# Performance work log

Hardware: AMD Instinct MI355X
Metric: run time of the kernel (lower is better)

The kernel has to match this reference:

```python
import jax, jax.numpy as jnp
import numpy as np
import math

B, C, H, W = 2, 256, 64, 64
E = 256           # embed_dim
AE = 64           # angle embed dim = embed_dim // 4
NH = 3            # num angle hypotheses
HEADS = 8
HALF = AE // 2    # 32 sin/cos frequencies

# 3x3 kernel tap grid (dy, dx), row-major, matching torchvision DeformConv2d tap order
KY = jnp.array([-1,-1,-1, 0,0,0, 1,1,1], jnp.float32)
KX = jnp.array([-1, 0, 1,-1,0,1,-1,0,1], jnp.float32)
# assumed angle hypothesis deltas around the predicted angle
HYPO_DELTAS = (-math.pi/12, 0.0, math.pi/12)


def conv2d(x, w, b, pad):
    y = jax.lax.conv_general_dilated(x, w, (1, 1), [(pad, pad), (pad, pad)],
                                     dimension_numbers=('NCHW', 'OIHW', 'NCHW'))
    return y + b[None, :, None, None]


def gen_offsets(angles):
    """Rotate the base 3x3 kernel taps by the per-pixel angle; offset = rotated - base.
    angles: (B, H*W, 1) -> offsets (B, 18, H, W), (dy,dx) interleaved per tap."""
    a = angles.reshape(-1, H, W)
    c = jnp.cos(a)[..., None]           # (B,H,W,1)
    s = jnp.sin(a)[..., None]
    ry = KX * s + KY * c                # rotated y of each tap, (B,H,W,9)
    rx = KX * c - KY * s                # rotated x
    off = jnp.stack([ry - KY, rx - KX], axis=-1)   # (B,H,W,9,2)
    return off.reshape(-1, H, W, 18).transpose(0, 3, 1, 2)


def deform_conv(x, offsets, w, b):
    """DeformConv2d k=3, stride=1, pad=1, dilation=1, zero padding outside.
    x (B,C,H,W), offsets (B,18,H,W), w (O,C,3,3)."""
    off = offsets.reshape(x.shape[0], 9, 2, H, W)
    oy = off[:, :, 0].transpose(0, 2, 3, 1)          # (B,H,W,9)
    ox = off[:, :, 1].transpose(0, 2, 3, 1)
    hh = jnp.arange(H, dtype=jnp.float32)[None, :, None, None]
    ww = jnp.arange(W, dtype=jnp.float32)[None, None, :, None]
    py = hh + KY + oy                                # sample y, (B,H,W,9)
    px = ww + KX + ox
    y0 = jnp.floor(py)
    x0 = jnp.floor(px)
    wy = (py - y0)[:, None]                          # (B,1,H,W,9)
    wx = (px - x0)[:, None]

    def gather(yi, xi):
        valid = (yi >= 0) & (yi <= H - 1) & (xi >= 0) & (xi <= W - 1)
        yc = jnp.clip(yi, 0, H - 1).astype(jnp.int32)
        xc = jnp.clip(xi, 0, W - 1).astype(jnp.int32)
        g = jax.vmap(lambda img, yy, xx: img[:, yy, xx])(x, yc, xc)  # (B,C,H,W,9)
        return g * valid[:, None].astype(x.dtype)

    samp = (gather(y0, x0) * (1 - wy) * (1 - wx)
            + gather(y0, x0 + 1) * (1 - wy) * wx
            + gather(y0 + 1, x0) * wy * (1 - wx)
            + gather(y0 + 1, x0 + 1) * wy * wx)      # (B,C,H,W,9)
    w9 = w.reshape(w.shape[0], w.shape[1], 9)
    return jnp.einsum('bchwk,ock->bohw', samp, w9) + b[None, :, None, None]


def angle_encode(angles, freq_mult, w1, b1, ln_g, ln_b, w2, b2):
    an = (angles / (math.pi / 2))[..., 0]                       # (B,HW) le90 norm
    dim_t = jnp.arange(HALF, dtype=jnp.float32) / HALF * math.pi
    ae = an[..., None] * (freq_mult * dim_t)                    # (B,HW,HALF)
    emb = jnp.concatenate([jnp.sin(ae), jnp.cos(ae)], axis=-1)  # (B,HW,AE)
    h = emb @ w1.T + b1
    mu = h.mean(-1, keepdims=True)
    var = h.var(-1, keepdims=True)
    h = (h - mu) * jax.lax.rsqrt(var + 1e-5) * ln_g + ln_b
    return jax.nn.relu(h) @ w2.T + b2


def mha(q, kv, in_w, in_b, out_w, out_b):
    # q (L,1,E), kv (L,NH,E); torch nn.MultiheadAttention math
    wq, wk, wv = jnp.split(in_w, 3, axis=0)
    bq, bk, bv = jnp.split(in_b, 3)
    hd = E // HEADS
    Q = (q @ wq.T + bq).reshape(-1, 1, HEADS, hd).transpose(0, 2, 1, 3)
    K = (kv @ wk.T + bk).reshape(-1, NH, HEADS, hd).transpose(0, 2, 1, 3)
    V = (kv @ wv.T + bv).reshape(-1, NH, HEADS, hd).transpose(0, 2, 1, 3)
    attn = jax.nn.softmax(jnp.einsum('lhqd,lhkd->lhqk', Q, K) / math.sqrt(hd), axis=-1)
    o = jnp.einsum('lhqk,lhkd->lhqd', attn, V).transpose(0, 2, 1, 3).reshape(-1, 1, E)
    return o @ out_w.T + out_b


def group_norm(x, g, b, groups=32, eps=1e-5):
    Bq, Cc, Hh, Ww = x.shape
    xg = x.reshape(Bq, groups, Cc // groups, Hh, Ww)
    mu = xg.mean((2, 3, 4), keepdims=True)
    var = xg.var((2, 3, 4), keepdims=True)
    xn = ((xg - mu) * jax.lax.rsqrt(var + eps)).reshape(x.shape)
    return xn * g[None, :, None, None] + b[None, :, None, None]


def setup_inputs() -> dict:
    key = jax.random.key(0)
    ks = iter(jax.random.split(key, 32))
    r = lambda *s: jax.random.normal(next(ks), s, jnp.float32) * 0.05
    z = lambda *s: jnp.zeros(s, jnp.float32)
    return {
        'features': jax.random.normal(next(ks), (B, C, H, W), jnp.float32),
        'ap_w1': r(C // 4, C, 3, 3), 'ap_b1': z(C // 4),
        'ap_w2': r(1, C // 4, 1, 1), 'ap_b2': z(1),
        'freq_mult': jnp.ones((HALF,), jnp.float32),
        'ae_w1': r(AE, AE), 'ae_b1': z(AE),
        'ae_ln_g': jnp.ones((AE,), jnp.float32), 'ae_ln_b': z(AE),
        'ae_w2': r(AE, AE), 'ae_b2': z(AE),
        'dc_w': r(E, C, 3, 3), 'dc_b': z(E),
        'attn_in_w': r(3 * E, E), 'attn_in_b': z(3 * E),
        'attn_out_w': r(E, E), 'attn_out_b': z(E),
        'ja_w1': r(E, E + AE, 1, 1), 'ja_b1': z(E),
        'ja_w2': r(E, E, 1, 1), 'ja_b2': z(E),
        'op_w1': r(E, E, 3, 3), 'op_b1': z(E),
        'gn_g': jnp.ones((E,), jnp.float32), 'gn_b': z(E),
        'op_w2': r(E, E, 1, 1), 'op_b2': z(E),
    }


def reference(features, ap_w1, ap_b1, ap_w2, ap_b2, freq_mult, ae_w1, ae_b1,
              ae_ln_g, ae_ln_b, ae_w2, ae_b2, dc_w, dc_b, attn_in_w, attn_in_b,
              attn_out_w, attn_out_b, ja_w1, ja_b1, ja_w2, ja_b2, op_w1, op_b1,
              gn_g, gn_b, op_w2, op_b2):
    # 1) angle prediction
    h1 = jax.nn.relu(conv2d(features, ap_w1, ap_b1, 1))
    angles = conv2d(h1, ap_w2, ap_b2, 0).reshape(B, H * W, 1)
    # 2) periodic angle encoding
    angle_embed = angle_encode(angles, freq_mult, ae_w1, ae_b1, ae_ln_g, ae_ln_b, ae_w2, ae_b2)
    # 3) rotation-aware deformable alignment
    aligned = deform_conv(features, gen_offsets(angles), dc_w, dc_b)
    # 4) multi-angle hypotheses fused by per-pixel attention
    cand = [deform_conv(features, gen_offsets(angles + d), dc_w, dc_b) for d in HYPO_DELTAS]
    feat_stack = jnp.stack(cand, axis=1)                       # (B,NH,E,H,W)
    q = aligned.transpose(0, 2, 3, 1).reshape(B * H * W, 1, E)
    kv = feat_stack.transpose(0, 3, 4, 1, 2).reshape(B * H * W, NH, E)
    fused = mha(q, kv, attn_in_w, attn_in_b, attn_out_w, attn_out_b)
    fused = fused.reshape(B, H, W, E).transpose(0, 3, 1, 2)
    # 5) joint angle-spatial attention gate
    ae_sp = angle_embed.reshape(B, H, W, AE).transpose(0, 3, 1, 2)
    ji = jnp.concatenate([fused, ae_sp], axis=1)
    gate = jax.nn.sigmoid(conv2d(jax.nn.relu(conv2d(ji, ja_w1, ja_b1, 0)), ja_w2, ja_b2, 0))
    enh = fused * gate + fused
    # 6) output projection
    o = jax.nn.relu(group_norm(conv2d(enh, op_w1, op_b1, 1), gn_g, gn_b))
    return conv2d(o, op_w2, op_b2, 0)
```

## Files before the change

kernel.cpp:

```cpp
#include <hip/hip_runtime.h>

#define PI_F 3.14159265358979323846f
#define HWSZ 4096
#define NPIX 8192

typedef __attribute__((ext_vector_type(8))) short short8;
typedef __attribute__((ext_vector_type(4))) short short4_t;
typedef __attribute__((ext_vector_type(4))) float f32x4;

__device__ __forceinline__ short f2bf(float x){
  unsigned u = __float_as_uint(x);
  unsigned r = (u + 0x7FFFu + ((u >> 16) & 1u)) >> 16;
  return (short)r;
}
__device__ __forceinline__ float bf2f(short v){
  return __uint_as_float(((unsigned)(unsigned short)v) << 16);
}

__device__ __forceinline__ float wsum64(float v){
  #pragma unroll
  for (int m = 32; m >= 1; m >>= 1) v += __shfl_xor(v, m, 64);
  return v;
}
__device__ __forceinline__ float wsum8(float v){
  v += __shfl_xor(v, 1, 64);
  v += __shfl_xor(v, 2, 64);
  v += __shfl_xor(v, 4, 64);
  return v;
}

__device__ __forceinline__ void gl_lds(const short* g, short* s){
  __builtin_amdgcn_global_load_lds(
      (const __attribute__((address_space(1))) unsigned int*)g,
      (__attribute__((address_space(3))) unsigned int*)s, 16, 0, 0);
}

__global__ void k_zero4(short* __restrict__ p, int n4){
  int i = blockIdx.x*256 + threadIdx.x;
  if (i < n4) ((short4_t*)p)[i] = (short4_t){0,0,0,0};
}

__global__ void k_nchw_split(const float* __restrict__ in, short* __restrict__ feat_bf,
    short* __restrict__ A3){
  __shared__ float tile[32][33];
  int b = blockIdx.z;
  int p0 = blockIdx.x * 32, c0 = blockIdx.y * 32;
  int tx = threadIdx.x, ty = threadIdx.y;
  #pragma unroll
  for (int i = ty; i < 32; i += 8)
    tile[i][tx] = in[((size_t)b*256 + c0 + i)*HWSZ + p0 + tx];
  __syncthreads();
  #pragma unroll
  for (int i = ty; i < 32; i += 8){
    float x = tile[tx][i];
    short hi = f2bf(x);
    short lo = f2bf(x - bf2f(hi));
    size_t p = (size_t)b*HWSZ + p0 + i;
    feat_bf[p*256 + c0 + tx] = hi;
    A3[p*768 + c0 + tx] = hi;
    A3[p*768 + 256 + c0 + tx] = hi;
    A3[p*768 + 512 + c0 + tx] = lo;
  }
}

__global__ void k_prep_tapw(const float* __restrict__ w, short* __restrict__ Bm){
  __shared__ short tile[9][256];
  int o = blockIdx.x;
  const float* wo = w + (size_t)o*2304;
  for (int i = threadIdx.x; i < 2304; i += 256){
    int c = i / 9, k = i - c*9;
    tile[k][c] = f2bf(wo[i]);
  }
  __syncthreads();
  for (int i = threadIdx.x; i < 2304; i += 256){
    int k = i >> 8, c = i & 255;
    Bm[((size_t)(k*256 + o))*256 + c] = tile[k][c];
  }
}

__global__ void k_prep_igw(const float* __restrict__ w, short* __restrict__ B2){
  __shared__ short tile[2304];
  int o = blockIdx.x;
  const float* wo = w + (size_t)o*2304;
  for (int i = threadIdx.x; i < 2304; i += 256){
    int c = i / 9, k = i - c*9;
    tile[k*256 + c] = f2bf(wo[i]);
  }
  __syncthreads();
  short* out = B2 + (size_t)o*2304;
  for (int i = threadIdx.x; i < 2304; i += 256) out[i] = tile[i];
}

__global__ void k_prep_apw3(const float* __restrict__ w, short* __restrict__ B3){
  int n = blockIdx.x, c = threadIdx.x;
  short hi = 0, lo = 0;
  if (n < 576){
    int o = n & 63, k = n >> 6;
    float x = w[((size_t)o*256 + c)*9 + k];
    hi = f2bf(x);
    lo = f2bf(x - bf2f(hi));
  }
  B3[(size_t)n*768 + c] = hi;
  B3[(size_t)n*768 + 256 + c] = lo;
  B3[(size_t)n*768 + 512 + c] = hi;
}

__global__ void k_castall(const float* __restrict__ s0, const float* __restrict__ s1,
    const float* __restrict__ s2, const float* __restrict__ s3, const float* __restrict__ s4,
    short* __restrict__ d0, short* __restrict__ d1, short* __restrict__ d2,
    short* __restrict__ d3, short* __restrict__ d4){
  int i = blockIdx.x*256 + threadIdx.x;
  if (i < 196608) d0[i] = f2bf(s0[i]);
  else if (i < 262144) d1[i-196608] = f2bf(s1[i-196608]);
  else if (i < 344064) d2[i-262144] = f2bf(s2[i-262144]);
  else if (i < 409600) d3[i-344064] = f2bf(s3[i-344064]);
  else if (i < 475136) d4[i-409600] = f2bf(s4[i-409600]);
}

template<int EPI, int BM>
__global__ __launch_bounds__(256) void k_gemml(const short* __restrict__ A,
    const short* __restrict__ B, void* __restrict__ Cv,
    const float* __restrict__ bias, const short* __restrict__ aux,
    int K, int ldc){
  constexpr int WM = BM/2;
  constexpr int AF = WM/16;
  __shared__ alignas(16) short sA[2][BM*32];
  __shared__ alignas(16) short sB[2][128*32];
  int tid = threadIdx.x;
  int w = tid >> 6, l = tid & 63;
  int wr = w & 1, wc = w >> 1;
  int ml = l & 15, g = l >> 4;
  int srow = tid >> 2;
  int sch = (tid & 3)*8;
  int m0 = blockIdx.x*BM, n0 = blockIdx.y*128;
  const short* Agp = A + (size_t)(m0 + srow)*K + sch;
  const short* Bgp = B + (size_t)(n0 + srow)*K + sch;
  short* sAd = &sA[0][srow*32 + sch];
  short* sBd = &sB[0][srow*32 + sch];
  f32x4 acc[AF][4];
  #pragma unroll
  for (int i = 0; i < AF; ++i)
    #pragma unroll
    for (int j = 0; j < 4; ++j) acc[i][j] = (f32x4){0.f,0.f,0.f,0.f};

  #define STAGE(bf, kt) { \
    _Pragma("unroll") \
    for (int c = 0; c < BM/64; ++c) \
      gl_lds(Agp + (size_t)(c*64)*K + (kt)*32, sAd + (bf)*BM*32 + c*2048); \
    _Pragma("unroll") \
    for (int c = 0; c < 2; ++c) \
      gl_lds(Bgp + (size_t)(c*64)*K + (kt)*32, sBd + (bf)*4096 + c*2048); \
  }
  int nk = K >> 5;
  STAGE(0, 0)
  int buf = 0;
  for (int kt = 0; kt < nk; ++kt){
    __syncthreads();
    if (kt + 1 < nk){ STAGE(buf^1, kt+1) }
    short8 af[AF], bq[4];
    #pragma unroll
    for (int i = 0; i < AF; ++i)
      af[i] = *(const short8*)&sA[buf][(wr*WM + i*16 + ml)*32 + g*8];
    #pragma unroll
    for (int j = 0; j < 4; ++j)
      bq[j] = *(const short8*)&sB[buf][(wc*64 + j*16 + ml)*32 + g*8];
    #pragma unroll
    for (int i = 0; i < AF; ++i)
      #pragma unroll
      for (int j = 0; j < 4; ++j)
        acc[i][j] = __builtin_amdgcn_mfma_f32_16x16x32_bf16(af[i], bq[j], acc[i][j], 0, 0, 0);
    buf ^= 1;
  }
  #undef STAGE

  int m0w = m0 + wr*WM;
  int n0w = n0 + wc*64;
  if constexpr (EPI == 4){
    __shared__ float cst[BM][129];
    #pragma unroll
    for (int fm = 0; fm < AF; ++fm)
      #pragma unroll
      for (int fn = 0; fn < 4; ++fn)
        #pragma unroll
        for (int r = 0; r < 4; ++r){
          int cl = wc*64 + fn*16 + ml;
          cst[wr*WM + fm*16 + g*4 + r][cl] = acc[fm][fn][r] + bias[blockIdx.y*128 + cl];
        }
    __syncthreads();
    int px0 = blockIdx.x*BM;
    int b = px0 >> 12, hw0 = px0 & 4095;
    int o = tid >> 1, seg = (tid & 1)*(BM/2);
    float* op = (float*)Cv + (((size_t)(b*256 + blockIdx.y*128 + o)) << 12) + hw0 + seg;
    #pragma unroll
    for (int i = 0; i < BM/2; i += 4){
      float4 vv = {cst[seg+i][o], cst[seg+i+1][o], cst[seg+i+2][o], cst[seg+i+3][o]};
      *(float4*)(op + i) = vv;
    }
  } else {
    #pragma unroll
    for (int fm = 0; fm < AF; ++fm)
      #pragma unroll
      for (int fn = 0; fn < 4; ++fn)
        #pragma unroll
        for (int r = 0; r < 4; ++r){
          int row = m0w + fm*16 + g*4 + r;
          int col = n0w + fn*16 + ml;
          float v = acc[fm][fn][r];
          if constexpr (EPI == 0){
            ((short*)Cv)[(size_t)row*ldc + col] = f2bf(v);
          } else if constexpr (EPI == 1){
            ((short*)Cv)[(size_t)row*ldc + col] = f2bf(v + bias[col]);
          } else if constexpr (EPI == 2){
            ((short*)Cv)[(size_t)row*ldc + col] = f2bf(fmaxf(v + bias[col], 0.f));
          } else if constexpr (EPI == 3){
            float f = bf2f(aux[(size_t)row*320 + col]);
            float s = 1.f/(1.f + __expf(-(v + bias[col])));
            ((short*)Cv)[(size_t)row*ldc + col] = f2bf(f * (1.f + s));
          } else if constexpr (EPI == 6){
            float f = bf2f(aux[(size_t)row*320 + col]);
            float s = 1.f/(1.f + __expf(-(v + bias[col])));
            int b = row >> 12, hw = row & 4095;
            int pi = b*4356 + ((hw>>6)+1)*66 + (hw&63) + 1;
            ((short*)Cv)[(size_t)pi*256 + col] = f2bf(f * (1.f + s));
          } else if constexpr (EPI == 7){
            ((short*)Cv)[(size_t)(col>>8)*2097152 + (size_t)row*256 + (col&255)] = f2bf(v);
          } else {
            ((float*)Cv)[(size_t)row*ldc + col] = v;
          }
        }
  }
}

__global__ __launch_bounds__(256) void k_igconv(const short* __restrict__ Xpad,
    const short* __restrict__ B2, float* __restrict__ PG){
  __shared__ alignas(16) short sA[2][64*32];
  __shared__ alignas(16) short sB[2][128*32];
  int zg = blockIdx.z;
  int tid = threadIdx.x;
  int w = tid >> 6, l = tid & 63;
  int wr = w & 1, wc = w >> 1;
  int ml = l & 15, g = l >> 4;
  int srow = tid >> 2;
  int sch = (tid & 3)*8;
  int m0 = blockIdx.x*64, n0 = blockIdx.y*128;
  int b = blockIdx.x >> 6, imgrow = blockIdx.x & 63;
  int qbase = b*4356 + (imgrow+1)*66 + srow + 1;
  const short* Bgp = B2 + (size_t)(n0 + srow)*2304 + zg*768 + sch;
  short* sAd = &sA[0][srow*32 + sch];
  short* sBd = &sB[0][srow*32 + sch];
  int toff[3];
  #pragma unroll
  for (int i = 0; i < 3; ++i){
    int t = zg*3 + i;
    toff[i] = (t/3 - 1)*66 + (t%3) - 1;
  }
  f32x4 acc[2][4];
  #pragma unroll
  for (int i = 0; i < 2; ++i)
    #pragma unroll
    for (int j = 0; j < 4; ++j) acc[i][j] = (f32x4){0.f,0.f,0.f,0.f};

  #define STG(bf, kt) { \
    int tap = (kt) >> 3, cofs = ((kt) & 7)*32; \
    gl_lds(Xpad + (size_t)(qbase + toff[tap])*256 + cofs + sch, sAd + (bf)*2048); \
    gl_lds(Bgp + (kt)*32, sBd + (bf)*4096); \
    gl_lds(Bgp + (size_t)64*2304 + (kt)*32, sBd + (bf)*4096 + 2048); \
  }
  STG(0, 0)
  int buf = 0;
  for (int kt = 0; kt < 24; ++kt){
    __syncthreads();
    if (kt < 23){ STG(buf^1, kt+1) }
    short8 af[2], bq[4];
    #pragma unroll
    for (int i = 0; i < 2; ++i)
      af[i] = *(const short8*)&sA[buf][(wr*32 + i*16 + ml)*32 + g*8];
    #pragma unroll
    for (int j = 0; j < 4; ++j)
      bq[j] = *(const short8*)&sB[buf][(wc*64 + j*16 + ml)*32 + g*8];
    #pragma unroll
    for (int i = 0; i < 2; ++i)
      #pragma unroll
      for (int j = 0; j < 4; ++j)
        acc[i][j] = __builtin_amdgcn_mfma_f32_16x16x32_bf16(af[i], bq[j], acc[i][j], 0, 0, 0);
    buf ^= 1;
  }
  #undef STG

  float* out = PG + (size_t)zg*2097152;
  int m0w = m0 + wr*32;
  int n0w = n0 + wc*64;
  #pragma unroll
  for (int fm = 0; fm < 2; ++fm)
    #pragma unroll
    for (int fn = 0; fn < 4; ++fn)
      #pragma unroll
      for (int r = 0; r < 4; ++r){
        int row = m0w + fm*16 + g*4 + r;
        int col = n0w + fn*16 + ml;
        out[(size_t)row*256 + col] = acc[fm][fn][r];
      }
}

__global__ void k_aph1enc(const float* __restrict__ T, const float* __restrict__ b1,
    const float* __restrict__ w2, const float* __restrict__ b2,
    const float* __restrict__ freq,
    const float* __restrict__ ew1, const float* __restrict__ eb1,
    const float* __restrict__ lng, const float* __restrict__ lnb,
    const float* __restrict__ ew2, const float* __restrict__ eb2,
    float* __restrict__ ang, short* __restrict__ gateA){
  const int KYi[9] = {-1,-1,-1,0,0,0,1,1,1};
  const int KXi[9] = {-1,0,1,-1,0,1,-1,0,1};
  int lane = threadIdx.x & 63;
  int p = blockIdx.x*4 + (threadIdx.x >> 6);
  int hw = p & 4095;
  int h = hw >> 6, w = hw & 63;
  float acc = b1[lane];
  #pragma unroll
  for (int k = 0; k < 9; ++k){
    int y = h + KYi[k], x = w + KXi[k];
    if (y < 0 || y > 63 || x < 0 || x > 63) continue;
    acc += T[(size_t)(p + KYi[k]*64 + KXi[k])*640 + k*64 + lane];
  }
  float av = wsum64(fmaxf(acc, 0.f) * w2[lane]) + b2[0];
  if (lane == 0) ang[p] = av;
  float an = av * (2.0f / PI_F);
  int f = lane & 31;
  float ph = an * freq[f] * ((float)f * (PI_F / 32.0f));
  float emb = (lane < 32) ? __sinf(ph) : __cosf(ph);
  float hh = eb1[lane];
  const float* w1r = ew1 + lane*64;
  #pragma unroll 8
  for (int i = 0; i < 64; ++i){
    float e = __shfl(emb, i, 64);
    hh = fmaf(e, w1r[i], hh);
  }
  float mu = wsum64(hh) * (1.0f/64.0f);
  float d = hh - mu;
  float var = wsum64(d*d) * (1.0f/64.0f);
  float hn = fmaf(d * rsqrtf(var + 1e-5f), lng[lane], lnb[lane]);
  float r = fmaxf(hn, 0.f);
  float o = eb2[lane];
  const float* w2r = ew2 + lane*64;
  #pragma unroll 8
  for (int i = 0; i < 64; ++i){
    float e = __shfl(r, i, 64);
    o = fmaf(e, w2r[i], o);
  }
  gateA[(size_t)p*320 + 256 + lane] = f2bf(o);
}

__global__ void k_meta(const float* __restrict__ ang, int2* __restrict__ moff,
    float4* __restrict__ mw){
  int i = blockIdx.x*256 + threadIdx.x;
  if (i >= NPIX*27) return;
  int p = i / 27;
  int j = i - p*27;
  int hyp = j / 9;
  int tap = j - hyp*9;
  float ky = (float)(tap/3 - 1), kx = (float)(tap - (tap/3)*3 - 1);
  float a = ang[p] + ((float)hyp - 1.0f) * (PI_F / 12.0f);
  float sn = __sinf(a), cs = __cosf(a);
  int b = p >> 12, hw = p & 4095;
  float py = (float)(hw >> 6) + kx*sn + ky*cs;
  float px = (float)(hw & 63) + kx*cs - ky*sn;
  float y0f = floorf(py), x0f = floorf(px);
  float wy = py - y0f, wx = px - x0f;
  int y0 = (int)y0f, x0 = (int)x0f;
  bool vx0 = (unsigned)x0 < 64u, vx1 = (unsigned)(x0+1) < 64u;
  bool vy0 = (unsigned)y0 < 64u, vy1 = (unsigned)(y0+1) < 64u;
  int xb = vx0 ? x0 : (vx1 ? x0+1 : 0);
  float sx0 = vx0 ? 1.f-wx : (vx1 ? wx : 0.f);
  float sx1 = (vx0 && vx1) ? wx : 0.f;
  int ry0 = vy0 ? y0 : 0;
  int ry1 = vy1 ? y0+1 : 0;
  float vw0 = vy0 ? 1.f-wy : 0.f;
  float vw1 = vy1 ? wy : 0.f;
  int base = (b << 12);
  moff[i] = make_int2(tap*4194304 + (base + ry0*64 + xb)*512,
                      tap*4194304 + (base + ry1*64 + xb)*512);
  mw[i] = make_float4(vw0*sx0, vw0*sx1, vw1*sx0, vw1*sx1);
}

__global__ __launch_bounds__(256, 4) void k_sample(const short* __restrict__ G,
    const int2* __restrict__ moff, const float4* __restrict__ mw,
    const float* __restrict__ bias, short* __restrict__ cand){
  __shared__ int2 smo[216];
  __shared__ float4 smw[216];
  int id = blockIdx.x;
  int sw = (id & 7)*128 + (id >> 3);
  int tid = threadIdx.x;
  int pbase = sw*8;
  if (tid < 216){
    smo[tid] = moff[pbase*27 + tid];
    smw[tid] = mw[pbase*27 + tid];
  }
  __syncthreads();
  int lp = (tid >> 6)*2 + ((tid >> 5) & 1);
  int p = pbase + lp;
  int c8 = (tid & 31)*8;
  float av[3][8];
  {
    float4 b0 = *(const float4*)(bias + c8);
    float4 b1 = *(const float4*)(bias + c8 + 4);
    #pragma unroll
    for (int h2 = 0; h2 < 3; ++h2){
      av[h2][0]=b0.x; av[h2][1]=b0.y; av[h2][2]=b0.z; av[h2][3]=b0.w;
      av[h2][4]=b1.x; av[h2][5]=b1.y; av[h2][6]=b1.z; av[h2][7]=b1.w;
    }
  }
  #pragma unroll
  for (int hyp = 0; hyp < 3; ++hyp){
    #pragma unroll 3
    for (int tap = 0; tap < 9; ++tap){
      int idx = lp*27 + hyp*9 + tap;
      int2 o = smo[idx];
      float4 wv = smw[idx];
      const short* r0 = (const short*)((const char*)G + o.x) + c8;
      const short* r1 = (const short*)((const char*)G + o.y) + c8;
      short8 v00 = *(const short8*)r0;
      short8 v01 = *(const short8*)(r0 + 256);
      short8 v10 = *(const short8*)r1;
      short8 v11 = *(const short8*)(r1 + 256);
      #pragma unroll
      for (int e = 0; e < 8; ++e){
        float s = wv.x*bf2f(v00[e]) + wv.y*bf2f(v01[e]);
        s += wv.z*bf2f(v10[e]) + wv.w*bf2f(v11[e]);
        av[hyp][e] += s;
      }
    }
  }
  #pragma unroll
  for (int hyp = 0; hyp < 3; ++hyp){
    short8 o;
    #pragma unroll
    for (int e = 0; e < 8; ++e) o[e] = f2bf(av[hyp][e]);
    *(short8*)(cand + ((size_t)hyp*NPIX + p)*256 + c8) = o;
  }
}

__global__ void k_attn(const short* __restrict__ Q, const short* __restrict__ KV,
    short* __restrict__ O){
  int lane = threadIdx.x & 63;
  int p = blockIdx.x*4 + (threadIdx.x >> 6);
  float q[4];
  { short4_t t = *(const short4_t*)(Q + (size_t)p*256 + lane*4);
    #pragma unroll
    for (int j = 0; j < 4; ++j) q[j] = bf2f(t[j]); }
  float kv[3][2][4];
  #pragma unroll
  for (int i = 0; i < 3; ++i){
    const short* rp = KV + (size_t)(i*NPIX + p)*512 + lane*4;
    short4_t kt = *(const short4_t*)rp;
    short4_t vt = *(const short4_t*)(rp + 256);
    #pragma unroll
    for (int j = 0; j < 4; ++j){ kv[i][0][j] = bf2f(kt[j]); kv[i][1][j] = bf2f(vt[j]); }
  }
  const float sc = 0.17677669529663688f;
  float s[3];
  #pragma unroll
  for (int i = 0; i < 3; ++i){
    float d = 0.f;
    #pragma unroll
    for (int j = 0; j < 4; ++j) d = fmaf(q[j], kv[i][0][j], d);
    s[i] = wsum8(d) * sc;
  }
  float m = fmaxf(s[0], fmaxf(s[1], s[2]));
  float e0 = __expf(s[0]-m), e1 = __expf(s[1]-m), e2 = __expf(s[2]-m);
  float inv = 1.f/(e0+e1+e2);
  short4_t ot;
  #pragma unroll
  for (int j = 0; j < 4; ++j)
    ot[j] = f2bf((e0*kv[0][1][j] + e1*kv[1][1][j] + e2*kv[2][1][j]) * inv);
  *(short4_t*)(O + (size_t)p*256 + lane*4) = ot;
}

__global__ void k_sum3stat(const float* __restrict__ PG, const float* __restrict__ bias,
    float* __restrict__ t, float* __restrict__ spart){
  int p0 = blockIdx.x * 8;
  int c = threadIdx.x;
  float bb = bias[c];
  float s = 0.f, s2 = 0.f;
  #pragma unroll
  for (int pp = 0; pp < 8; ++pp){
    size_t idx = (size_t)(p0+pp)*256 + c;
    float v = PG[idx] + PG[idx + 2097152] + PG[idx + 4194304] + bb;
    t[idx] = v;
    s += v; s2 = fmaf(v, v, s2);
  }
  s  += __shfl_xor(s, 1, 64);  s  += __shfl_xor(s, 2, 64);  s  += __shfl_xor(s, 4, 64);
  s2 += __shfl_xor(s2, 1, 64); s2 += __shfl_xor(s2, 2, 64); s2 += __shfl_xor(s2, 4, 64);
  if ((c & 7) == 0){
    int b = p0 >> 12;
    int bg = b*32 + (c >> 3);
    int blk = blockIdx.x & 511;
    spart[(size_t)(bg*512 + blk)*2]     = s;
    spart[(size_t)(bg*512 + blk)*2 + 1] = s2;
  }
}

__global__ void k_gnfin(const float* __restrict__ spart, float* __restrict__ stat){
  int bg = blockIdx.x;
  const float* sp = spart + (size_t)bg*1024;
  float s = 0.f, s2 = 0.f;
  for (int i = threadIdx.x; i < 512; i += 256){
    s += sp[i*2]; s2 += sp[i*2+1];
  }
  s = wsum64(s); s2 = wsum64(s2);
  __shared__ float rs[4], rs2[4];
  int wid = threadIdx.x >> 6;
  if ((threadIdx.x & 63) == 0){ rs[wid] = s; rs2[wid] = s2; }
  __syncthreads();
  if (threadIdx.x == 0){
    float S = rs[0]+rs[1]+rs[2]+rs[3];
    float S2 = rs2[0]+rs2[1]+rs2[2]+rs2[3];
    float mean = S * (1.f/32768.f);
    float var = S2 * (1.f/32768.f) - mean*mean;
    stat[bg*2]   = mean;
    stat[bg*2+1] = rsqrtf(var + 1e-5f);
  }
}

__global__ void k_gnrelu(const float* __restrict__ t, const float* __restrict__ stat,
    const float* __restrict__ gng, const float* __restrict__ gnb,
    short* __restrict__ a){
  int p = blockIdx.x*4 + (threadIdx.x >> 6);
  int c4 = (threadIdx.x & 63)*4;
  int b = p >> 12, g = c4 >> 3;
  float mean = stat[(b*32+g)*2], rstd = stat[(b*32+g)*2+1];
  float4 gg = *(const float4*)(gng + c4);
  float4 bb = *(const float4*)(gnb + c4);
  float4 v = *(const float4*)(t + (size_t)p*256 + c4);
  short4_t o;
  o[0] = f2bf(fmaxf((v.x - mean)*rstd*gg.x + bb.x, 0.f));
  o[1] = f2bf(fmaxf((v.y - mean)*rstd*gg.y + bb.y, 0.f));
  o[2] = f2bf(fmaxf((v.z - mean)*rstd*gg.z + bb.z, 0.f));
  o[3] = f2bf(fmaxf((v.w - mean)*rstd*gg.w + bb.w, 0.f));
  *(short4_t*)(a + (size_t)p*256 + c4) = o;
}

extern "C" void kernel_launch(void* const* d_in, const int* in_sizes, int n_in,
                              void* d_out, int out_size, void* d_ws, size_t ws_size,
                              hipStream_t stream){
  (void)in_sizes; (void)n_in; (void)out_size; (void)ws_size;
  const float* features   = (const float*)d_in[0];
  const float* ap_w1      = (const float*)d_in[1];
  const float* ap_b1      = (const float*)d_in[2];
  const float* ap_w2      = (const float*)d_in[3];
  const float* ap_b2      = (const float*)d_in[4];
  const float* freq       = (const float*)d_in[5];
  const float* ae_w1      = (const float*)d_in[6];
  const float* ae_b1      = (const float*)d_in[7];
  const float* ae_ln_g    = (const float*)d_in[8];
  const float* ae_ln_b    = (const float*)d_in[9];
  const float* ae_w2      = (const float*)d_in[10];
  const float* ae_b2      = (const float*)d_in[11];
  const float* dc_w       = (const float*)d_in[12];
  const float* dc_b       = (const float*)d_in[13];
  const float* attn_in_w  = (const float*)d_in[14];
  const float* attn_in_b  = (const float*)d_in[15];
  const float* attn_out_w = (const float*)d_in[16];
  const float* attn_out_b = (const float*)d_in[17];
  const float* ja_w1      = (const float*)d_in[18];
  const float* ja_b1      = (const float*)d_in[19];
  const float* ja_w2      = (const float*)d_in[20];
  const float* ja_b2      = (const float*)d_in[21];
  const float* op_w1      = (const float*)d_in[22];
  const float* op_b1      = (const float*)d_in[23];
  const float* gn_g       = (const float*)d_in[24];
  const float* gn_b       = (const float*)d_in[25];
  const float* op_w2      = (const float*)d_in[26];
  const float* op_b2      = (const float*)d_in[27];

  char* base = (char*)d_ws;
  #define ALLOC(ty, name, elems) ty* name = (ty*)base; base += (size_t)(elems)*sizeof(ty);
  ALLOC(short, feat_bf, 8192*256)
  ALLOC(short, Bdc,     2304*256)
  ALLOC(short, B2op,    256*2304)
  ALLOC(short, B3ap,    640*768)
  ALLOC(short, inw_bf,  768*256)
  ALLOC(short, wot_bf,  256*256)
  ALLOC(short, jw1_bf,  256*320)
  ALLOC(short, jw2_bf,  256*256)
  ALLOC(short, wop2_bf, 256*256)
  ALLOC(short, Gbuf,    24576*768)
  ALLOC(short, gguard,  64)
  ALLOC(short, cand_bf, 3*8192*256)
  ALLOC(short, O_bf,    8192*256)
  ALLOC(short, gateA,   8192*320)
  ALLOC(short, hid_bf,  8192*256)
  ALLOC(short, enh_pad, 2*4356*256)
  ALLOC(float, angbuf,  8192)
  ALLOC(float, tbuf,    8192*256)
  ALLOC(float, gstat,   128)
  ALLOC(float, spart,   65536)
  ALLOC(short, a_bf,    8192*256)
  ALLOC(int,   moffb,   2*NPIX*27)
  ALLOC(float, mwb,     4*NPIX*27)
  #undef ALLOC
  (void)gguard;
  short* A3 = cand_bf;
  float* T_ap = (float*)Gbuf;
  short* KVbuf = Gbuf;
  short* Qbuf  = Gbuf + (size_t)24576*512;
  float* PG    = (float*)Gbuf;
  int2*  moff  = (int2*)moffb;
  float4* mwv  = (float4*)mwb;

  dim3 t32(32, 8);
  k_zero4<<<2178, 256, 0, stream>>>(enh_pad, 557568);
  k_nchw_split<<<dim3(128,8,2), t32, 0, stream>>>(features, feat_bf, A3);
  k_prep_tapw<<<256, 256, 0, stream>>>(dc_w,  Bdc);
  k_prep_igw<<<256, 256, 0, stream>>>(op_w1, B2op);
  k_prep_apw3<<<640, 256, 0, stream>>>(ap_w1, B3ap);
  k_castall<<<1856, 256, 0, stream>>>(attn_in_w, attn_out_w, ja_w1, ja_w2, op_w2,
                                      inw_bf, wot_bf, jw1_bf, jw2_bf, wop2_bf);

  k_gemml<5,64><<<dim3(128,5), 256, 0, stream>>>(A3, B3ap, T_ap, nullptr, nullptr, 768, 640);
  k_aph1enc<<<2048, 256, 0, stream>>>(T_ap, ap_b1, ap_w2, ap_b2, freq,
                                      ae_w1, ae_b1, ae_ln_g, ae_ln_b, ae_w2, ae_b2,
                                      angbuf, gateA);
  k_meta<<<864, 256, 0, stream>>>(angbuf, moff, mwv);
  k_gemml<7,128><<<dim3(64,18), 256, 0, stream>>>(feat_bf, Bdc, Gbuf, nullptr, nullptr, 256, 2304);
  k_sample<<<1024, 256, 0, stream>>>(Gbuf, moff, mwv, dc_b, cand_bf);
  k_gemml<1,128><<<dim3(192,4), 256, 0, stream>>>(cand_bf, inw_bf + (size_t)256*256, KVbuf,
                                                  attn_in_b + 256, nullptr, 256, 512);
  k_gemml<1,64><<<dim3(128,2), 256, 0, stream>>>(cand_bf + (size_t)NPIX*256, inw_bf, Qbuf,
                                                 attn_in_b, nullptr, 256, 256);
  k_attn<<<2048, 256, 0, stream>>>(Qbuf, KVbuf, O_bf);
  k_gemml<1,64><<<dim3(128,2), 256, 0, stream>>>(O_bf, wot_bf, gateA, attn_out_b, nullptr, 256, 320);
  k_gemml<2,64><<<dim3(128,2), 256, 0, stream>>>(gateA, jw1_bf, hid_bf, ja_b1, nullptr, 320, 256);
  k_gemml<6,64><<<dim3(128,2), 256, 0, stream>>>(hid_bf, jw2_bf, enh_pad, ja_b2, gateA, 256, 256);
  k_igconv<<<dim3(128,2,3), 256, 0, stream>>>(enh_pad, B2op, PG);
  k_sum3stat<<<1024, 256, 0, stream>>>(PG, op_b1, tbuf, spart);
  k_gnfin<<<64, 256, 0, stream>>>(spart, gstat);
  k_gnrelu<<<2048, 256, 0, stream>>>(tbuf, gstat, gn_g, gn_b, a_bf);
  k_gemml<4,64><<<dim3(128,2), 256, 0, stream>>>(a_bf, wop2_bf, (float*)d_out, op_b2, nullptr, 256, 256);
}
```

Baseline: 218.9 us.

## Merge prep kernels, fuse meta into encoder, shrink angle GEMM K, retile small GEMMs

Five weight-prep and zeroing kernels become one launch, and the per-pixel offset/weight metadata computation moves into the angle-encoder kernel so the angle buffer round trip and one launch go away. The angle-predictor GEMM drops from a three-term to a two-term split-bf16 product (hi*hi + lo*hi), which shrinks K from 768 to 512. The small N=256 GEMMs use a 64-wide N tile to double the block count for better occupancy. Dropping the hi*lo term lowers the precision of the predicted angle, and that loss carries into the sampling offsets.

```diff
diff --git a/kernel.cpp b/kernel.cpp
--- a/kernel.cpp
+++ b/kernel.cpp
@@ -35,9 +35,57 @@
       (__attribute__((address_space(3))) unsigned int*)s, 16, 0, 0);
 }
 
-__global__ void k_zero4(short* __restrict__ p, int n4){
-  int i = blockIdx.x*256 + threadIdx.x;
-  if (i < n4) ((short4_t*)p)[i] = (short4_t){0,0,0,0};
+__global__ void k_prep(const float* __restrict__ dc_w, const float* __restrict__ op_w1,
+    const float* __restrict__ ap_w1,
+    const float* __restrict__ s0, const float* __restrict__ s1,
+    const float* __restrict__ s2, const float* __restrict__ s3, const float* __restrict__ s4,
+    short* __restrict__ enh_pad, short* __restrict__ Bdc, short* __restrict__ B2op,
+    short* __restrict__ B3, short* __restrict__ d0, short* __restrict__ d1,
+    short* __restrict__ d2, short* __restrict__ d3, short* __restrict__ d4){
+  __shared__ short tile[2304];
+  int bx = blockIdx.x, tid = threadIdx.x;
+  if (bx < 2178){
+    int i = bx*256 + tid;
+    if (i < 557568) ((short4_t*)enh_pad)[i] = (short4_t){0,0,0,0};
+  } else if (bx < 2434){
+    int o = bx - 2178;
+    const float* wo = dc_w + (size_t)o*2304;
+    for (int i = tid; i < 2304; i += 256){
+      int c = i / 9, k = i - c*9;
+      tile[k*256 + c] = f2bf(wo[i]);
+    }
+    __syncthreads();
+    for (int i = tid; i < 2304; i += 256){
+      int k = i >> 8, c = i & 255;
+      Bdc[((size_t)(k*256 + o))*256 + c] = tile[i];
+    }
+  } else if (bx < 2690){
+    int o = bx - 2434;
+    const float* wo = op_w1 + (size_t)o*2304;
+    for (int i = tid; i < 2304; i += 256){
+      int c = i / 9, k = i - c*9;
+      tile[k*256 + c] = f2bf(wo[i]);
+    }
+    __syncthreads();
+    short* out = B2op + (size_t)o*2304;
+    for (int i = tid; i < 2304; i += 256) out[i] = tile[i];
+  } else if (bx < 3330){
+    int n = bx - 2690, c = tid;
+    short hi = 0;
+    if (n < 576){
+      int o = n & 63, k = n >> 6;
+      hi = f2bf(ap_w1[((size_t)o*256 + c)*9 + k]);
+    }
+    B3[(size_t)n*512 + c] = hi;
+    B3[(size_t)n*512 + 256 + c] = hi;
+  } else {
+    int i = (bx - 3330)*256 + tid;
+    if (i < 196608) d0[i] = f2bf(s0[i]);
+    else if (i < 262144) d1[i-196608] = f2bf(s1[i-196608]);
+    else if (i < 344064) d2[i-262144] = f2bf(s2[i-262144]);
+    else if (i < 409600) d3[i-344064] = f2bf(s3[i-344064]);
+    else if (i < 475136) d4[i-409600] = f2bf(s4[i-409600]);
+  }
 }
 
 __global__ void k_nchw_split(const float* __restrict__ in, short* __restrict__ feat_bf,
@@ -57,82 +105,29 @@
     short lo = f2bf(x - bf2f(hi));
     size_t p = (size_t)b*HWSZ + p0 + i;
     feat_bf[p*256 + c0 + tx] = hi;
-    A3[p*768 + c0 + tx] = hi;
-    A3[p*768 + 256 + c0 + tx] = hi;
-    A3[p*768 + 512 + c0 + tx] = lo;
-  }
-}
-
-__global__ void k_prep_tapw(const float* __restrict__ w, short* __restrict__ Bm){
-  __shared__ short tile[9][256];
-  int o = blockIdx.x;
-  const float* wo = w + (size_t)o*2304;
-  for (int i = threadIdx.x; i < 2304; i += 256){
-    int c = i / 9, k = i - c*9;
-    tile[k][c] = f2bf(wo[i]);
-  }
-  __syncthreads();
-  for (int i = threadIdx.x; i < 2304; i += 256){
-    int k = i >> 8, c = i & 255;
-    Bm[((size_t)(k*256 + o))*256 + c] = tile[k][c];
-  }
-}
-
-__global__ void k_prep_igw(const float* __restrict__ w, short* __restrict__ B2){
-  __shared__ short tile[2304];
-  int o = blockIdx.x;
-  const float* wo = w + (size_t)o*2304;
-  for (int i = threadIdx.x; i < 2304; i += 256){
-    int c = i / 9, k = i - c*9;
-    tile[k*256 + c] = f2bf(wo[i]);
-  }
-  __syncthreads();
-  short* out = B2 + (size_t)o*2304;
-  for (int i = threadIdx.x; i < 2304; i += 256) out[i] = tile[i];
-}
-
-__global__ void k_prep_apw3(const float* __restrict__ w, short* __restrict__ B3){
-  int n = blockIdx.x, c = threadIdx.x;
-  short hi = 0, lo = 0;
-  if (n < 576){
-    int o = n & 63, k = n >> 6;
-    float x = w[((size_t)o*256 + c)*9 + k];
-    hi = f2bf(x);
-    lo = f2bf(x - bf2f(hi));
-  }
-  B3[(size_t)n*768 + c] = hi;
-  B3[(size_t)n*768 + 256 + c] = lo;
-  B3[(size_t)n*768 + 512 + c] = hi;
-}
-
-__global__ void k_castall(const float* __restrict__ s0, const float* __restrict__ s1,
-    const float* __restrict__ s2, const float* __restrict__ s3, const float* __restrict__ s4,
-    short* __restrict__ d0, short* __restrict__ d1, short* __restrict__ d2,
-    short* __restrict__ d3, short* __restrict__ d4){
-  int i = blockIdx.x*256 + threadIdx.x;
-  if (i < 196608) d0[i] = f2bf(s0[i]);
-  else if (i < 262144) d1[i-196608] = f2bf(s1[i-196608]);
-  else if (i < 344064) d2[i-262144] = f2bf(s2[i-262144]);
-  else if (i < 409600) d3[i-344064] = f2bf(s3[i-344064]);
-  else if (i < 475136) d4[i-409600] = f2bf(s4[i-409600]);
-}
-
-template<int EPI, int BM>
+    A3[p*512 + c0 + tx] = hi;
+    A3[p*512 + 256 + c0 + tx] = lo;
+  }
+}
+
+template<int EPI, int BM, int BN = 128>
 __global__ __launch_bounds__(256) void k_gemml(const short* __restrict__ A,
     const short* __restrict__ B, void* __restrict__ Cv,
     const float* __restrict__ bias, const short* __restrict__ aux,
     int K, int ldc){
-  constexpr int WM = BM/2;
+  constexpr int NWC = BN/64;
+  constexpr int NWR = 4/NWC;
+  constexpr int WM = BM/NWR;
   constexpr int AF = WM/16;
   __shared__ alignas(16) short sA[2][BM*32];
-  __shared__ alignas(16) short sB[2][128*32];
+  __shared__ alignas(16) short sB[2][BN*32];
   int tid = threadIdx.x;
   int w = tid >> 6, l = tid & 63;
-  int wr = w & 1, wc = w >> 1;
+  int wc = w % NWC, wr = w / NWC;
   int ml = l & 15, g = l >> 4;
   int srow = tid >> 2;
   int sch = (tid & 3)*8;
-  int m0 = blockIdx.x*BM, n0 = blockIdx.y*128;
+  int m0 = blockIdx.x*BM, n0 = blockIdx.y*BN;
   const short* Agp = A + (size_t)(m0 + srow)*K + sch;
   const short* Bgp = B + (size_t)(n0 + srow)*K + sch;
   short* sAd = &sA[0][srow*32 + sch];
@@ -148,8 +143,8 @@
     for (int c = 0; c < BM/64; ++c) \
       gl_lds(Agp + (size_t)(c*64)*K + (kt)*32, sAd + (bf)*BM*32 + c*2048); \
     _Pragma("unroll") \
-    for (int c = 0; c < 2; ++c) \
-      gl_lds(Bgp + (size_t)(c*64)*K + (kt)*32, sBd + (bf)*4096 + c*2048); \
+    for (int c = 0; c < BN/64; ++c) \
+      gl_lds(Bgp + (size_t)(c*64)*K + (kt)*32, sBd + (bf)*BN*32 + c*2048); \
   }
   int nk = K >> 5;
   STAGE(0, 0)
@@ -308,11 +303,13 @@
     const float* __restrict__ ew1, const float* __restrict__ eb1,
     const float* __restrict__ lng, const float* __restrict__ lnb,
     const float* __restrict__ ew2, const float* __restrict__ eb2,
-    float* __restrict__ ang, short* __restrict__ gateA){
+    short* __restrict__ gateA, int2* __restrict__ moff, float4* __restrict__ mw){
   const int KYi[9] = {-1,-1,-1,0,0,0,1,1,1};
   const int KXi[9] = {-1,0,1,-1,0,1,-1,0,1};
+  __shared__ float sang[4];
   int lane = threadIdx.x & 63;
-  int p = blockIdx.x*4 + (threadIdx.x >> 6);
+  int wid = threadIdx.x >> 6;
+  int p = blockIdx.x*4 + wid;
   int hw = p & 4095;
   int h = hw >> 6, w = hw & 63;
   float acc = b1[lane];
@@ -323,7 +320,7 @@
     acc += T[(size_t)(p + KYi[k]*64 + KXi[k])*640 + k*64 + lane];
   }
   float av = wsum64(fmaxf(acc, 0.f) * w2[lane]) + b2[0];
-  if (lane == 0) ang[p] = av;
+  if (lane == 0) sang[wid] = av;
   float an = av * (2.0f / PI_F);
   int f = lane & 31;
   float ph = an * freq[f] * ((float)f * (PI_F / 32.0f));
@@ -348,38 +345,38 @@
     o = fmaf(e, w2r[i], o);
   }
   gateA[(size_t)p*320 + 256 + lane] = f2bf(o);
-}
-
-__global__ void k_meta(const float* __restrict__ ang, int2* __restrict__ moff,
-    float4* __restrict__ mw){
-  int i = blockIdx.x*256 + threadIdx.x;
-  if (i >= NPIX*27) return;
-  int p = i / 27;
-  int j = i - p*27;
-  int hyp = j / 9;
-  int tap = j - hyp*9;
-  float ky = (float)(tap/3 - 1), kx = (float)(tap - (tap/3)*3 - 1);
-  float a = ang[p] + ((float)hyp - 1.0f) * (PI_F / 12.0f);
-  float sn = __sinf(a), cs = __cosf(a);
-  int b = p >> 12, hw = p & 4095;
-  float py = (float)(hw >> 6) + kx*sn + ky*cs;
-  float px = (float)(hw & 63) + kx*cs - ky*sn;
-  float y0f = floorf(py), x0f = floorf(px);
-  float wy = py - y0f, wx = px - x0f;
-  int y0 = (int)y0f, x0 = (int)x0f;
-  bool vx0 = (unsigned)x0 < 64u, vx1 = (unsigned)(x0+1) < 64u;
-  bool vy0 = (unsigned)y0 < 64u, vy1 = (unsigned)(y0+1) < 64u;
-  int xb = vx0 ? x0 : (vx1 ? x0+1 : 0);
-  float sx0 = vx0 ? 1.f-wx : (vx1 ? wx : 0.f);
-  float sx1 = (vx0 && vx1) ? wx : 0.f;
-  int ry0 = vy0 ? y0 : 0;
-  int ry1 = vy1 ? y0+1 : 0;
-  float vw0 = vy0 ? 1.f-wy : 0.f;
-  float vw1 = vy1 ? wy : 0.f;
-  int base = (b << 12);
-  moff[i] = make_int2(tap*4194304 + (base + ry0*64 + xb)*512,
-                      tap*4194304 + (base + ry1*64 + xb)*512);
-  mw[i] = make_float4(vw0*sx0, vw0*sx1, vw1*sx0, vw1*sx1);
+  __syncthreads();
+  int tid = threadIdx.x;
+  if (tid < 108){
+    int lp = tid / 27;
+    int j = tid - lp*27;
+    int pp = blockIdx.x*4 + lp;
+    int hyp = j / 9;
+    int tap = j - hyp*9;
+    float ky = (float)(tap/3 - 1), kx = (float)(tap - (tap/3)*3 - 1);
+    float a = sang[lp] + ((float)hyp - 1.0f) * (PI_F / 12.0f);
+    float sn = __sinf(a), cs = __cosf(a);
+    int b2i = pp >> 12, hw2 = pp & 4095;
+    float py = (float)(hw2 >> 6) + kx*sn + ky*cs;
+    float px = (float)(hw2 & 63) + kx*cs - ky*sn;
+    float y0f = floorf(py), x0f = floorf(px);
+    float wy = py - y0f, wx = px - x0f;
+    int y0 = (int)y0f, x0 = (int)x0f;
+    bool vx0 = (unsigned)x0 < 64u, vx1 = (unsigned)(x0+1) < 64u;
+    bool vy0 = (unsigned)y0 < 64u, vy1 = (unsigned)(y0+1) < 64u;
+    int xb = vx0 ? x0 : (vx1 ? x0+1 : 0);
+    float sx0 = vx0 ? 1.f-wx : (vx1 ? wx : 0.f);
+    float sx1 = (vx0 && vx1) ? wx : 0.f;
+    int ry0 = vy0 ? y0 : 0;
+    int ry1 = vy1 ? y0+1 : 0;
+    float vw0 = vy0 ? 1.f-wy : 0.f;
+    float vw1 = vy1 ? wy : 0.f;
+    int base = (b2i << 12);
+    int mi = pp*27 + j;
+    moff[mi] = make_int2(tap*4194304 + (base + ry0*64 + xb)*512,
+                         tap*4194304 + (base + ry1*64 + xb)*512);
+    mw[mi] = make_float4(vw0*sx0, vw0*sx1, vw1*sx0, vw1*sx1);
+  }
 }
 
 __global__ __launch_bounds__(256, 4) void k_sample(const short* __restrict__ G,
@@ -577,7 +574,7 @@
   ALLOC(short, feat_bf, 8192*256)
   ALLOC(short, Bdc,     2304*256)
   ALLOC(short, B2op,    256*2304)
-  ALLOC(short, B3ap,    640*768)
+  ALLOC(short, B3ap,    640*512)
   ALLOC(short, inw_bf,  768*256)
   ALLOC(short, wot_bf,  256*256)
   ALLOC(short, jw1_bf,  256*320)
@@ -590,7 +587,6 @@
   ALLOC(short, gateA,   8192*320)
   ALLOC(short, hid_bf,  8192*256)
   ALLOC(short, enh_pad, 2*4356*256)
-  ALLOC(float, angbuf,  8192)
   ALLOC(float, tbuf,    8192*256)
   ALLOC(float, gstat,   128)
   ALLOC(float, spart,   65536)
@@ -608,29 +604,25 @@
   float4* mwv  = (float4*)mwb;
 
   dim3 t32(32, 8);
-  k_zero4<<<2178, 256, 0, stream>>>(enh_pad, 557568);
+  k_prep<<<5186, 256, 0, stream>>>(dc_w, op_w1, ap_w1,
+      attn_in_w, attn_out_w, ja_w1, ja_w2, op_w2,
+      enh_pad, Bdc, B2op, B3ap, inw_bf, wot_bf, jw1_bf, jw2_bf, wop2_bf);
   k_nchw_split<<<dim3(128,8,2), t32, 0, stream>>>(features, feat_bf, A3);
-  k_prep_tapw<<<256, 256, 0, stream>>>(dc_w,  Bdc);
-  k_prep_igw<<<256, 256, 0, stream>>>(op_w1, B2op);
-  k_prep_apw3<<<640, 256, 0, stream>>>(ap_w1, B3ap);
-  k_castall<<<1856, 256, 0, stream>>>(attn_in_w, attn_out_w, ja_w1, ja_w2, op_w2,
-                                      inw_bf, wot_bf, jw1_bf, jw2_bf, wop2_bf);
-
-  k_gemml<5,64><<<dim3(128,5), 256, 0, stream>>>(A3, B3ap, T_ap, nullptr, nullptr, 768, 640);
+
+  k_gemml<5,64><<<dim3(128,5), 256, 0, stream>>>(A3, B3ap, T_ap, nullptr, nullptr, 512, 640);
   k_aph1enc<<<2048, 256, 0, stream>>>(T_ap, ap_b1, ap_w2, ap_b2, freq,
                                       ae_w1, ae_b1, ae_ln_g, ae_ln_b, ae_w2, ae_b2,
-                                      angbuf, gateA);
-  k_meta<<<864, 256, 0, stream>>>(angbuf, moff, mwv);
+                                      gateA, moff, mwv);
   k_gemml<7,128><<<dim3(64,18), 256, 0, stream>>>(feat_bf, Bdc, Gbuf, nullptr, nullptr, 256, 2304);
   k_sample<<<1024, 256, 0, stream>>>(Gbuf, moff, mwv, dc_b, cand_bf);
   k_gemml<1,128><<<dim3(192,4), 256, 0, stream>>>(cand_bf, inw_bf + (size_t)256*256, KVbuf,
                                                   attn_in_b + 256, nullptr, 256, 512);
-  k_gemml<1,64><<<dim3(128,2), 256, 0, stream>>>(cand_bf + (size_t)NPIX*256, inw_bf, Qbuf,
-                                                 attn_in_b, nullptr, 256, 256);
+  k_gemml<1,64,64><<<dim3(128,4), 256, 0, stream>>>(cand_bf + (size_t)NPIX*256, inw_bf, Qbuf,
+                                                    attn_in_b, nullptr, 256, 256);
   k_attn<<<2048, 256, 0, stream>>>(Qbuf, KVbuf, O_bf);
-  k_gemml<1,64><<<dim3(128,2), 256, 0, stream>>>(O_bf, wot_bf, gateA, attn_out_b, nullptr, 256, 320);
-  k_gemml<2,64><<<dim3(128,2), 256, 0, stream>>>(gateA, jw1_bf, hid_bf, ja_b1, nullptr, 320, 256);
-  k_gemml<6,64><<<dim3(128,2), 256, 0, stream>>>(hid_bf, jw2_bf, enh_pad, ja_b2, gateA, 256, 256);
+  k_gemml<1,64,64><<<dim3(128,4), 256, 0, stream>>>(O_bf, wot_bf, gateA, attn_out_b, nullptr, 256, 320);
+  k_gemml<2,64,64><<<dim3(128,4), 256, 0, stream>>>(gateA, jw1_bf, hid_bf, ja_b1, nullptr, 320, 256);
+  k_gemml<6,64,64><<<dim3(128,4), 256, 0, stream>>>(hid_bf, jw2_bf, enh_pad, ja_b2, gateA, 256, 256);
   k_igconv<<<dim3(128,2,3), 256, 0, stream>>>(enh_pad, B2op, PG);
   k_sum3stat<<<1024, 256, 0, stream>>>(PG, op_b1, tbuf, spart);
   k_gnfin<<<64, 256, 0, stream>>>(spart, gstat);
```

Result: faster. 197.7 us (-9.7%).
